# Kernel optimization log

Measured on AMD Instinct MI355X. Metric: run time of the kernel, lower is better.

The kernel has to match this reference:

```python
import jax, jax.numpy as jnp
import numpy as np

N_FRAMES = 500000
INPUT_LEN = 128
N_MEMORY = 64
N_CLASSES = 64


def setup_inputs() -> dict:
    key = jax.random.key(0)
    ks = jax.random.split(key, 8)
    return {
        "inputs": jax.random.normal(ks[0], (N_FRAMES, INPUT_LEN), dtype=jnp.float32),
        "targets": jax.random.randint(ks[1], (N_FRAMES,), 0, N_CLASSES, dtype=jnp.int32),
        "W_left": jax.random.normal(ks[2], (INPUT_LEN, N_MEMORY), dtype=jnp.float32) * 0.05,
        "b_left": jax.random.normal(ks[3], (N_MEMORY,), dtype=jnp.float32) * 0.05,
        "W_right": jax.random.normal(ks[4], (INPUT_LEN, N_MEMORY), dtype=jnp.float32) * 0.05,
        "b_right": jax.random.normal(ks[5], (N_MEMORY,), dtype=jnp.float32) * 0.05,
        "W_logit": jax.random.normal(ks[6], (N_MEMORY, N_CLASSES), dtype=jnp.float32) * 0.05,
        "b_logit": jax.random.normal(ks[7], (N_CLASSES,), dtype=jnp.float32) * 0.05,
    }


def reference(inputs, targets, W_left, b_left, W_right, b_right, W_logit, b_logit):
    # inputs: [T, input_len]; targets unused by forward (consumed by external CTC loss)
    left = jax.nn.sigmoid(inputs @ W_left + b_left)    # [T, M]
    right = jax.nn.sigmoid(inputs @ W_right + b_right)  # [T, M]
    prod = left * right                                  # [T, M]

    # Linear recurrence: u_0 = 0; u_t = prod[t-1] * u_{t-1} + (1 - left[t-1])
    a = prod[:-1]        # [T-1, M]
    b = 1.0 - left[:-1]  # [T-1, M]

    def step(u, ab):
        a_t, b_t = ab
        u = a_t * u + b_t
        return u, u

    u0 = jnp.zeros((left.shape[1],), dtype=left.dtype)
    _, zs = jax.lax.scan(step, u0, (a, b))
    z = jnp.concatenate([u0[None, :], zs], axis=0)  # [T, M]

    logits = z @ W_logit + b_logit  # [T, n_classes]
    return logits
```

## Files before the change

### kernel.cpp

```cpp
#include <hip/hip_runtime.h>
#include <hip/hip_fp16.h>


constexpr int NF  = 500000;
constexpr int KIN = 128;
constexpr int M   = 64;
constexpr int CH  = 64;
constexpr int NC  = (NF + CH - 1) / CH;
constexpr int NG  = (NC + 63) / 64;
constexpr int GPW = (NG + 3) / 4;

typedef _Float16 f16x8 __attribute__((ext_vector_type(8)));
typedef __fp16   fp16x2 __attribute__((ext_vector_type(2)));
typedef float    f32x4 __attribute__((ext_vector_type(4)));

__device__ __forceinline__ float sig(float x) {
    return __builtin_amdgcn_rcpf(1.0f + __expf(-x));
}

__global__ void k0_pack(const float* __restrict__ WL, const float* __restrict__ WR,
                        const float* __restrict__ WLog,
                        _Float16* __restrict__ wpre, _Float16* __restrict__ wlogpre)
{
    int flat = blockIdx.x * 1024 + threadIdx.x * 4;
    if (flat < 16384) {
        int k = flat >> 7, col = flat & 127;
        float4 v = (col < 64) ? *(const float4*)&WL[k * 64 + col]
                              : *(const float4*)&WR[k * 64 + (col - 64)];
        int kb = k >> 3, kj = k & 7;
        wpre[(kb * 128 + col + 0) * 8 + kj] = (_Float16)v.x;
        wpre[(kb * 128 + col + 1) * 8 + kj] = (_Float16)v.y;
        wpre[(kb * 128 + col + 2) * 8 + kj] = (_Float16)v.z;
        wpre[(kb * 128 + col + 3) * 8 + kj] = (_Float16)v.w;
    } else if (flat < 16384 + 4096) {
        int f2 = flat - 16384;
        int k = f2 >> 6, c = f2 & 63;
        float4 v = *(const float4*)&WLog[f2];
        int kb = k >> 3, kj = k & 7;
        wlogpre[(kb * 64 + c + 0) * 8 + kj] = (_Float16)v.x;
        wlogpre[(kb * 64 + c + 1) * 8 + kj] = (_Float16)v.y;
        wlogpre[(kb * 64 + c + 2) * 8 + kj] = (_Float16)v.z;
        wlogpre[(kb * 64 + c + 3) * 8 + kj] = (_Float16)v.w;
    }
}

__global__ __launch_bounds__(256, 4)
void k1_prefix(const float* __restrict__ X, const _Float16* __restrict__ wpre,
               const float* __restrict__ bL, const float* __restrict__ bR,
               float* __restrict__ sA, float* __restrict__ sB,
               _Float16* __restrict__ pre)
{
    __shared__ _Float16 w_s[16384];
    __shared__ float pA_s[256], pB_s[256];
    const int tid = threadIdx.x, lane = tid & 63, w = tid >> 6;
    const int arow = lane & 15, kb = lane >> 4;
    const int t0 = blockIdx.x * CH;

    #pragma unroll
    for (int i = 0; i < 8; ++i) {
        int c16 = i * 256 + tid;
        *(f16x8*)&w_s[c16 * 8] = ((const f16x8*)wpre)[c16];
    }
    __syncthreads();

    f32x4 acc[8];
    #pragma unroll
    for (int c = 0; c < 8; ++c) acc[c] = (f32x4){0.f, 0.f, 0.f, 0.f};
    {
        const int xrow = t0 + w * 16 + arow;
        const float* xp = X + (size_t)xrow * KIN;
        const bool rowok = xrow < NF;
        #pragma unroll
        for (int s = 0; s < 4; ++s) {
            f32x4 v0 = (f32x4){0.f, 0.f, 0.f, 0.f}, v1 = v0;
            if (rowok) {
                v0 = *(const f32x4*)&xp[s * 32 + kb * 8];
                v1 = *(const f32x4*)&xp[s * 32 + kb * 8 + 4];
            }
            fp16x2 p0 = __builtin_amdgcn_cvt_pkrtz(v0.x, v0.y);
            fp16x2 p1 = __builtin_amdgcn_cvt_pkrtz(v0.z, v0.w);
            fp16x2 p2 = __builtin_amdgcn_cvt_pkrtz(v1.x, v1.y);
            fp16x2 p3 = __builtin_amdgcn_cvt_pkrtz(v1.z, v1.w);
            f16x8 af = { (_Float16)p0[0], (_Float16)p0[1],
                         (_Float16)p1[0], (_Float16)p1[1],
                         (_Float16)p2[0], (_Float16)p2[1],
                         (_Float16)p3[0], (_Float16)p3[1] };
            #pragma unroll
            for (int c = 0; c < 8; ++c) {
                f16x8 bf = *(const f16x8*)&w_s[((s * 4 + kb) * 128 + c * 16 + arow) * 8];
                acc[c] = __builtin_amdgcn_mfma_f32_16x16x32_f16(af, bf, acc[c], 0, 0, 0);
            }
        }
    }

    float a[4][4], b[4][4];
    #pragma unroll
    for (int c = 0; c < 4; ++c) {
        float blv = bL[c * 16 + arow], brv = bR[c * 16 + arow];
        #pragma unroll
        for (int reg = 0; reg < 4; ++reg) {
            float lv = sig(acc[c][reg] + blv);
            float rv = sig(acc[c + 4][reg] + brv);
            a[c][reg] = lv * rv;
            b[c][reg] = 1.0f - lv;
        }
    }

    float Ai[4], Bi[4];
    #pragma unroll
    for (int c = 0; c < 4; ++c) {
        float A = 1.f, B = 0.f;
        #pragma unroll
        for (int reg = 0; reg < 4; ++reg) {
            if (t0 + w * 16 + kb * 4 + reg < NF - 1) {
                B = fmaf(a[c][reg], B, b[c][reg]);
                A *= a[c][reg];
            }
        }
        Ai[c] = A; Bi[c] = B;
    }
    #pragma unroll
    for (int d = 16; d < 64; d <<= 1) {
        #pragma unroll
        for (int c = 0; c < 4; ++c) {
            float pA = __shfl_up(Ai[c], d), pB = __shfl_up(Bi[c], d);
            if (lane >= d) { Bi[c] = fmaf(Ai[c], pB, Bi[c]); Ai[c] *= pA; }
        }
    }

    float eA[4], eB[4];
    #pragma unroll
    for (int c = 0; c < 4; ++c) {
        eA[c] = __shfl_up(Ai[c], 16);
        eB[c] = __shfl_up(Bi[c], 16);
        if (kb == 0) { eA[c] = 1.f; eB[c] = 0.f; }
    }
    if (kb == 3) {
        #pragma unroll
        for (int c = 0; c < 4; ++c) {
            pA_s[w * 64 + c * 16 + arow] = Ai[c];
            pB_s[w * 64 + c * 16 + arow] = Bi[c];
        }
    }
    __syncthreads();

    float EA[4] = {1.f, 1.f, 1.f, 1.f}, EB[4] = {0.f, 0.f, 0.f, 0.f};
    for (int s2 = 0; s2 < w; ++s2) {
        #pragma unroll
        for (int c = 0; c < 4; ++c) {
            float qa = pA_s[s2 * 64 + c * 16 + arow];
            float qb = pB_s[s2 * 64 + c * 16 + arow];
            EB[c] = fmaf(qa, EB[c], qb);
            EA[c] *= qa;
        }
    }
    _Float16* prebase = pre + (size_t)blockIdx.x * 8192;
    #pragma unroll
    for (int c = 0; c < 4; ++c) {
        float pa = eA[c] * EA[c];
        float pb = fmaf(eA[c], EB[c], eB[c]);
        f16x8 sv;
        #pragma unroll
        for (int reg = 0; reg < 4; ++reg) {
            fp16x2 pp = __builtin_amdgcn_cvt_pkrtz(pa, pb);
            sv[2 * reg]     = (_Float16)pp[0];
            sv[2 * reg + 1] = (_Float16)pp[1];
            if (t0 + w * 16 + kb * 4 + reg < NF - 1) {
                pb = fmaf(a[c][reg], pb, b[c][reg]);
                pa *= a[c][reg];
            }
        }
        *(f16x8*)&prebase[((((w * 4 + kb) * 4 + c) * 16 + arow) * 4) * 2] = sv;
    }
    if (tid < 64) {
        float At = 1.f, Bt = 0.f;
        #pragma unroll
        for (int s2 = 0; s2 < 4; ++s2) {
            float qa = pA_s[s2 * 64 + tid], qb = pB_s[s2 * 64 + tid];
            Bt = fmaf(qa, Bt, qb);
            At *= qa;
        }
        sA[tid * NC + blockIdx.x] = At;
        sB[tid * NC + blockIdx.x] = Bt;
    }
}

__global__ __launch_bounds__(256)
void k3_scan(const float* __restrict__ sA, const float* __restrict__ sB,
             float* __restrict__ u0)
{
    __shared__ float tA_s[4], tB_s[4];
    const int j    = blockIdx.x;
    const int lane = threadIdx.x & 63;
    const int w    = threadIdx.x >> 6;

    float PA[GPW], PB[GPW];
    float cA = 1.f, cB = 0.f;
    #pragma unroll
    for (int g = 0; g < GPW; ++g) {
        int c = (w * GPW + g) * 64 + lane;
        float A = 1.f, B = 0.f;
        if (c < NC) { A = sA[j * NC + c]; B = sB[j * NC + c]; }
        #pragma unroll
        for (int d = 1; d < 64; d <<= 1) {
            float pA = __shfl_up(A, d), pB = __shfl_up(B, d);
            if (lane >= d) { B = fmaf(A, pB, B); A *= pA; }
        }
        float eA = __shfl_up(A, 1), eB = __shfl_up(B, 1);
        if (lane == 0) { eA = 1.f; eB = 0.f; }
        PA[g] = eA * cA;
        PB[g] = fmaf(eA, cB, eB);
        float tA = __shfl(A, 63), tB = __shfl(B, 63);
        cB = fmaf(tA, cB, tB);
        cA *= tA;
    }
    if (lane == 0) { tA_s[w] = cA; tB_s[w] = cB; }
    __syncthreads();
    float uw = 0.f;
    for (int s2 = 0; s2 < w; ++s2) uw = fmaf(tA_s[s2], uw, tB_s[s2]);
    #pragma unroll
    for (int g = 0; g < GPW; ++g) {
        int c = (w * GPW + g) * 64 + lane;
        if (c < NC) u0[c * M + j] = fmaf(PA[g], uw, PB[g]);
    }
}

__global__ __launch_bounds__(256, 8)
void k4_light(const _Float16* __restrict__ pre, const float* __restrict__ u0,
              const _Float16* __restrict__ wlogpre, const float* __restrict__ bLog,
              float* __restrict__ out)
{
    __shared__ _Float16 z_s[64 * 72];
    const int tid = threadIdx.x, lane = tid & 63, w = tid >> 6;
    const int arow = lane & 15, kb = lane >> 4;
    const int t0 = blockIdx.x * CH;

    float u0v[4];
    #pragma unroll
    for (int c = 0; c < 4; ++c) u0v[c] = u0[blockIdx.x * 64 + c * 16 + arow];

    const _Float16* prebase = pre + (size_t)blockIdx.x * 8192;
    #pragma unroll
    for (int c = 0; c < 4; ++c) {
        f16x8 pv = *(const f16x8*)&prebase[((((w * 4 + kb) * 4 + c) * 16 + arow) * 4) * 2];
        #pragma unroll
        for (int reg = 0; reg < 4; ++reg) {
            int rl = w * 16 + kb * 4 + reg;
            float z = fmaf((float)pv[2 * reg], u0v[c], (float)pv[2 * reg + 1]);
            z_s[rl * 72 + c * 16 + arow] = (_Float16)z;
        }
    }
    __syncthreads();

    f32x4 acc2[4];
    #pragma unroll
    for (int ct = 0; ct < 4; ++ct) acc2[ct] = (f32x4){0.f, 0.f, 0.f, 0.f};
    #pragma unroll
    for (int ks = 0; ks < 2; ++ks) {
        f16x8 af = *(const f16x8*)&z_s[(w * 16 + arow) * 72 + ks * 32 + kb * 8];
        #pragma unroll
        for (int ct = 0; ct < 4; ++ct) {
            f16x8 bf = *(const f16x8*)&wlogpre[((ks * 4 + kb) * 64 + ct * 16 + arow) * 8];
            acc2[ct] = __builtin_amdgcn_mfma_f32_16x16x32_f16(af, bf, acc2[ct], 0, 0, 0);
        }
    }
    #pragma unroll
    for (int ct = 0; ct < 4; ++ct) {
        float bv = bLog[ct * 16 + arow];
        #pragma unroll
        for (int reg = 0; reg < 4; ++reg) {
            int t = t0 + w * 16 + kb * 4 + reg;
            if (t < NF)
                __builtin_nontemporal_store(acc2[ct][reg] + bv,
                                            &out[t * M + ct * 16 + arow]);
        }
    }
}

extern "C" void kernel_launch(void* const* d_in, const int* in_sizes, int n_in,
                              void* d_out, int out_size, void* d_ws, size_t ws_size,
                              hipStream_t stream)
{
    const float* X    = (const float*)d_in[0];
    const float* WL   = (const float*)d_in[2];
    const float* bL   = (const float*)d_in[3];
    const float* WR   = (const float*)d_in[4];
    const float* bR   = (const float*)d_in[5];
    const float* WLog = (const float*)d_in[6];
    const float* bLog = (const float*)d_in[7];

    _Float16* pre = (_Float16*)d_ws;
    float* sA = (float*)((char*)d_ws + (size_t)NC * 8192 * 2);
    float* sB = sA + (size_t)64 * NC;
    float* u0 = sB + (size_t)64 * NC;
    _Float16* wpre    = (_Float16*)(u0 + (size_t)64 * NC);
    _Float16* wlogpre = wpre + 16384;

    k0_pack<<<20, 256, 0, stream>>>(WL, WR, WLog, wpre, wlogpre);
    k1_prefix<<<NC, 256, 0, stream>>>(X, wpre, bL, bR, sA, sB, pre);
    k3_scan<<<M, 256, 0, stream>>>(sA, sB, u0);
    k4_light<<<NC, 256, 0, stream>>>(pre, u0, wlogpre, bLog, (float*)d_out);
}
```

Before: 164.3 us.

## Make k1_prefix persistent with register prefetch of next chunk's inputs

k1_prefix now launches a fixed grid of 1024 blocks that loop over chunks in grid-stride fashion. The fp16 weight tile is loaded into LDS once per block instead of once per chunk. Each iteration prefetches the next chunk's X rows into registers while the sigmoid and scan work runs, to hide global load latency. A trailing __syncthreads is added per iteration, and k4 now reads the prefix data with nontemporal loads; register pressure rises from the held prefetch buffer.

Result: faster. 159.4 us (-3.0%).

```diff
diff --git a/kernel.cpp b/kernel.cpp
--- a/kernel.cpp
+++ b/kernel.cpp
@@ -9,6 +9,7 @@
 constexpr int NC  = (NF + CH - 1) / CH;
 constexpr int NG  = (NC + 63) / 64;
 constexpr int GPW = (NG + 3) / 4;
+constexpr int K1GRID = 1024;
 
 typedef _Float16 f16x8 __attribute__((ext_vector_type(8)));
 typedef __fp16   fp16x2 __attribute__((ext_vector_type(2)));
@@ -54,7 +55,6 @@
     __shared__ float pA_s[256], pB_s[256];
     const int tid = threadIdx.x, lane = tid & 63, w = tid >> 6;
     const int arow = lane & 15, kb = lane >> 4;
-    const int t0 = blockIdx.x * CH;
 
     #pragma unroll
     for (int i = 0; i < 8; ++i) {
@@ -63,24 +63,38 @@
     }
     __syncthreads();
 
-    f32x4 acc[8];
-    #pragma unroll
-    for (int c = 0; c < 8; ++c) acc[c] = (f32x4){0.f, 0.f, 0.f, 0.f};
+    float blv[4], brv[4];
+    #pragma unroll
+    for (int c = 0; c < 4; ++c) { blv[c] = bL[c * 16 + arow]; brv[c] = bR[c * 16 + arow]; }
+
+    f32x4 xv[8];
+    int cid = blockIdx.x;
     {
-        const int xrow = t0 + w * 16 + arow;
+        const int xrow = cid * CH + w * 16 + arow;
         const float* xp = X + (size_t)xrow * KIN;
         const bool rowok = xrow < NF;
         #pragma unroll
         for (int s = 0; s < 4; ++s) {
-            f32x4 v0 = (f32x4){0.f, 0.f, 0.f, 0.f}, v1 = v0;
-            if (rowok) {
-                v0 = *(const f32x4*)&xp[s * 32 + kb * 8];
-                v1 = *(const f32x4*)&xp[s * 32 + kb * 8 + 4];
-            }
-            fp16x2 p0 = __builtin_amdgcn_cvt_pkrtz(v0.x, v0.y);
-            fp16x2 p1 = __builtin_amdgcn_cvt_pkrtz(v0.z, v0.w);
-            fp16x2 p2 = __builtin_amdgcn_cvt_pkrtz(v1.x, v1.y);
-            fp16x2 p3 = __builtin_amdgcn_cvt_pkrtz(v1.z, v1.w);
+            xv[2 * s]     = rowok ? *(const f32x4*)&xp[s * 32 + kb * 8]
+                                  : (f32x4){0.f, 0.f, 0.f, 0.f};
+            xv[2 * s + 1] = rowok ? *(const f32x4*)&xp[s * 32 + kb * 8 + 4]
+                                  : (f32x4){0.f, 0.f, 0.f, 0.f};
+        }
+    }
+
+    while (cid < NC) {
+        const int t0 = cid * CH;
+        const int nxt = cid + K1GRID;
+
+        f32x4 acc[8];
+        #pragma unroll
+        for (int c = 0; c < 8; ++c) acc[c] = (f32x4){0.f, 0.f, 0.f, 0.f};
+        #pragma unroll
+        for (int s = 0; s < 4; ++s) {
+            fp16x2 p0 = __builtin_amdgcn_cvt_pkrtz(xv[2 * s].x, xv[2 * s].y);
+            fp16x2 p1 = __builtin_amdgcn_cvt_pkrtz(xv[2 * s].z, xv[2 * s].w);
+            fp16x2 p2 = __builtin_amdgcn_cvt_pkrtz(xv[2 * s + 1].x, xv[2 * s + 1].y);
+            fp16x2 p3 = __builtin_amdgcn_cvt_pkrtz(xv[2 * s + 1].z, xv[2 * s + 1].w);
             f16x8 af = { (_Float16)p0[0], (_Float16)p0[1],
                          (_Float16)p1[0], (_Float16)p1[1],
                          (_Float16)p2[0], (_Float16)p2[1],
@@ -91,97 +105,111 @@
                 acc[c] = __builtin_amdgcn_mfma_f32_16x16x32_f16(af, bf, acc[c], 0, 0, 0);
             }
         }
-    }
-
-    float a[4][4], b[4][4];
-    #pragma unroll
-    for (int c = 0; c < 4; ++c) {
-        float blv = bL[c * 16 + arow], brv = bR[c * 16 + arow];
-        #pragma unroll
-        for (int reg = 0; reg < 4; ++reg) {
-            float lv = sig(acc[c][reg] + blv);
-            float rv = sig(acc[c + 4][reg] + brv);
-            a[c][reg] = lv * rv;
-            b[c][reg] = 1.0f - lv;
-        }
-    }
-
-    float Ai[4], Bi[4];
-    #pragma unroll
-    for (int c = 0; c < 4; ++c) {
-        float A = 1.f, B = 0.f;
-        #pragma unroll
-        for (int reg = 0; reg < 4; ++reg) {
-            if (t0 + w * 16 + kb * 4 + reg < NF - 1) {
-                B = fmaf(a[c][reg], B, b[c][reg]);
-                A *= a[c][reg];
-            }
-        }
-        Ai[c] = A; Bi[c] = B;
-    }
-    #pragma unroll
-    for (int d = 16; d < 64; d <<= 1) {
+
+        if (nxt < NC) {
+            const int xrow = nxt * CH + w * 16 + arow;
+            const float* xp = X + (size_t)xrow * KIN;
+            const bool rowok = xrow < NF;
+            #pragma unroll
+            for (int s = 0; s < 4; ++s) {
+                xv[2 * s]     = rowok ? *(const f32x4*)&xp[s * 32 + kb * 8]
+                                      : (f32x4){0.f, 0.f, 0.f, 0.f};
+                xv[2 * s + 1] = rowok ? *(const f32x4*)&xp[s * 32 + kb * 8 + 4]
+                                      : (f32x4){0.f, 0.f, 0.f, 0.f};
+            }
+        }
+
+        float a[4][4], b[4][4];
         #pragma unroll
         for (int c = 0; c < 4; ++c) {
-            float pA = __shfl_up(Ai[c], d), pB = __shfl_up(Bi[c], d);
-            if (lane >= d) { Bi[c] = fmaf(Ai[c], pB, Bi[c]); Ai[c] *= pA; }
-        }
-    }
-
-    float eA[4], eB[4];
-    #pragma unroll
-    for (int c = 0; c < 4; ++c) {
-        eA[c] = __shfl_up(Ai[c], 16);
-        eB[c] = __shfl_up(Bi[c], 16);
-        if (kb == 0) { eA[c] = 1.f; eB[c] = 0.f; }
-    }
-    if (kb == 3) {
+            #pragma unroll
+            for (int reg = 0; reg < 4; ++reg) {
+                float lv = sig(acc[c][reg] + blv[c]);
+                float rv = sig(acc[c + 4][reg] + brv[c]);
+                a[c][reg] = lv * rv;
+                b[c][reg] = 1.0f - lv;
+            }
+        }
+
+        float Ai[4], Bi[4];
         #pragma unroll
         for (int c = 0; c < 4; ++c) {
-            pA_s[w * 64 + c * 16 + arow] = Ai[c];
-            pB_s[w * 64 + c * 16 + arow] = Bi[c];
-        }
-    }
-    __syncthreads();
-
-    float EA[4] = {1.f, 1.f, 1.f, 1.f}, EB[4] = {0.f, 0.f, 0.f, 0.f};
-    for (int s2 = 0; s2 < w; ++s2) {
+            float A = 1.f, B = 0.f;
+            #pragma unroll
+            for (int reg = 0; reg < 4; ++reg) {
+                if (t0 + w * 16 + kb * 4 + reg < NF - 1) {
+                    B = fmaf(a[c][reg], B, b[c][reg]);
+                    A *= a[c][reg];
+                }
+            }
+            Ai[c] = A; Bi[c] = B;
+        }
+        #pragma unroll
+        for (int d = 16; d < 64; d <<= 1) {
+            #pragma unroll
+            for (int c = 0; c < 4; ++c) {
+                float pA = __shfl_up(Ai[c], d), pB = __shfl_up(Bi[c], d);
+                if (lane >= d) { Bi[c] = fmaf(Ai[c], pB, Bi[c]); Ai[c] *= pA; }
+            }
+        }
+
+        float eA[4], eB[4];
         #pragma unroll
         for (int c = 0; c < 4; ++c) {
-            float qa = pA_s[s2 * 64 + c * 16 + arow];
-            float qb = pB_s[s2 * 64 + c * 16 + arow];
-            EB[c] = fmaf(qa, EB[c], qb);
-            EA[c] *= qa;
-        }
-    }
-    _Float16* prebase = pre + (size_t)blockIdx.x * 8192;
-    #pragma unroll
-    for (int c = 0; c < 4; ++c) {
-        float pa = eA[c] * EA[c];
-        float pb = fmaf(eA[c], EB[c], eB[c]);
-        f16x8 sv;
-        #pragma unroll
-        for (int reg = 0; reg < 4; ++reg) {
-            fp16x2 pp = __builtin_amdgcn_cvt_pkrtz(pa, pb);
-            sv[2 * reg]     = (_Float16)pp[0];
-            sv[2 * reg + 1] = (_Float16)pp[1];
-            if (t0 + w * 16 + kb * 4 + reg < NF - 1) {
-                pb = fmaf(a[c][reg], pb, b[c][reg]);
-                pa *= a[c][reg];
-            }
-        }
-        *(f16x8*)&prebase[((((w * 4 + kb) * 4 + c) * 16 + arow) * 4) * 2] = sv;
-    }
-    if (tid < 64) {
-        float At = 1.f, Bt = 0.f;
-        #pragma unroll
-        for (int s2 = 0; s2 < 4; ++s2) {
-            float qa = pA_s[s2 * 64 + tid], qb = pB_s[s2 * 64 + tid];
-            Bt = fmaf(qa, Bt, qb);
-            At *= qa;
-        }
-        sA[tid * NC + blockIdx.x] = At;
-        sB[tid * NC + blockIdx.x] = Bt;
+            eA[c] = __shfl_up(Ai[c], 16);
+            eB[c] = __shfl_up(Bi[c], 16);
+            if (kb == 0) { eA[c] = 1.f; eB[c] = 0.f; }
+        }
+        if (kb == 3) {
+            #pragma unroll
+            for (int c = 0; c < 4; ++c) {
+                pA_s[w * 64 + c * 16 + arow] = Ai[c];
+                pB_s[w * 64 + c * 16 + arow] = Bi[c];
+            }
+        }
+        __syncthreads();
+
+        float EA[4] = {1.f, 1.f, 1.f, 1.f}, EB[4] = {0.f, 0.f, 0.f, 0.f};
+        for (int s2 = 0; s2 < w; ++s2) {
+            #pragma unroll
+            for (int c = 0; c < 4; ++c) {
+                float qa = pA_s[s2 * 64 + c * 16 + arow];
+                float qb = pB_s[s2 * 64 + c * 16 + arow];
+                EB[c] = fmaf(qa, EB[c], qb);
+                EA[c] *= qa;
+            }
+        }
+        _Float16* prebase = pre + (size_t)cid * 8192;
+        #pragma unroll
+        for (int c = 0; c < 4; ++c) {
+            float pa = eA[c] * EA[c];
+            float pb = fmaf(eA[c], EB[c], eB[c]);
+            f16x8 sv;
+            #pragma unroll
+            for (int reg = 0; reg < 4; ++reg) {
+                fp16x2 pp = __builtin_amdgcn_cvt_pkrtz(pa, pb);
+                sv[2 * reg]     = (_Float16)pp[0];
+                sv[2 * reg + 1] = (_Float16)pp[1];
+                if (t0 + w * 16 + kb * 4 + reg < NF - 1) {
+                    pb = fmaf(a[c][reg], pb, b[c][reg]);
+                    pa *= a[c][reg];
+                }
+            }
+            *(f16x8*)&prebase[((((w * 4 + kb) * 4 + c) * 16 + arow) * 4) * 2] = sv;
+        }
+        if (tid < 64) {
+            float At = 1.f, Bt = 0.f;
+            #pragma unroll
+            for (int s2 = 0; s2 < 4; ++s2) {
+                float qa = pA_s[s2 * 64 + tid], qb = pB_s[s2 * 64 + tid];
+                Bt = fmaf(qa, Bt, qb);
+                At *= qa;
+            }
+            sA[tid * NC + cid] = At;
+            sB[tid * NC + cid] = Bt;
+        }
+        __syncthreads();
+        cid = nxt;
     }
 }
 
@@ -242,7 +270,8 @@
     const _Float16* prebase = pre + (size_t)blockIdx.x * 8192;
     #pragma unroll
     for (int c = 0; c < 4; ++c) {
-        f16x8 pv = *(const f16x8*)&prebase[((((w * 4 + kb) * 4 + c) * 16 + arow) * 4) * 2];
+        f16x8 pv = __builtin_nontemporal_load(
+            (const f16x8*)&prebase[((((w * 4 + kb) * 4 + c) * 16 + arow) * 4) * 2]);
         #pragma unroll
         for (int reg = 0; reg < 4; ++reg) {
             int rl = w * 16 + kb * 4 + reg;
@@ -297,7 +326,7 @@
     _Float16* wlogpre = wpre + 16384;
 
     k0_pack<<<20, 256, 0, stream>>>(WL, WR, WLog, wpre, wlogpre);
-    k1_prefix<<<NC, 256, 0, stream>>>(X, wpre, bL, bR, sA, sB, pre);
+    k1_prefix<<<K1GRID, 256, 0, stream>>>(X, wpre, bL, bR, sA, sB, pre);
     k3_scan<<<M, 256, 0, stream>>>(sA, sB, u0);
     k4_light<<<NC, 256, 0, stream>>>(pre, u0, wlogpre, bLog, (float*)d_out);
 }
```
